# Optimization experiments

Hardware: AMD Instinct MI355X
Metric: run time of the kernel (lower is better)

Reference implementation:

```python
import jax, jax.numpy as jnp
import numpy as np

LN_EPS = 1e-5


def setup_inputs() -> dict:
    key = jax.random.key(0)
    ks = jax.random.split(key, 4)
    B, N, C, K = 512, 100, 256, 3
    query = jax.random.normal(ks[0], (B, N, C), dtype=jnp.float32)
    value = jax.random.normal(ks[1], (B, N, C), dtype=jnp.float32)
    # nn.Linear(C, N+K): weight stored as [out,in] in torch; here use [in,out]
    W_wl = jax.random.normal(ks[2], (C, N + K), dtype=jnp.float32) / np.sqrt(C)
    b_wl = jax.random.normal(ks[3], (N + K,), dtype=jnp.float32) * 0.01
    ln_gamma = jnp.ones((C,), dtype=jnp.float32)
    ln_beta = jnp.zeros((C,), dtype=jnp.float32)
    return {"query": query, "value": value, "W_wl": W_wl, "b_wl": b_wl,
            "ln_gamma": ln_gamma, "ln_beta": ln_beta}


def reference(query, value, W_wl, b_wl, ln_gamma, ln_beta):
    B, N, C = query.shape
    K = W_wl.shape[1] - N
    # dynamic conv weights from query: [B, N, K] depthwise + [B, N, N] pointwise
    dy = jnp.einsum('bnc,ck->bnk', query, W_wl) + b_wl
    dw = dy[:, :, :K]          # depthwise kernels, one per (b, proposal)
    pw = dy[:, :, K:]          # pointwise mixing matrix [B, N, N]
    # depthwise conv1d along C with 'same' padding (cross-correlation like torch)
    pad_l = (K - 1) // 2
    pad_r = K - 1 - pad_l
    vp = jnp.pad(value, ((0, 0), (0, 0), (pad_l, pad_r)))
    depth = jnp.zeros_like(value)
    for k in range(K):  # K is tiny (3): static unrolled loop
        depth = depth + dw[:, :, k:k + 1] * vp[:, :, k:k + C]
    depth = jax.nn.relu(depth)
    # pointwise conv (kernel size 1) == per-sample NxN mix over proposals
    out = jnp.einsum('bnm,bmc->bnc', pw, depth)
    # LayerNorm over C
    mu = jnp.mean(out, axis=-1, keepdims=True)
    var = jnp.var(out, axis=-1, keepdims=True)
    out = (out - mu) * jax.lax.rsqrt(var + LN_EPS) * ln_gamma + ln_beta
    return out
```

## Files before the change

### kernel.cpp

```cpp
#include <hip/hip_runtime.h>

#define NN 100
#define CC 256
#define NKK 103
#define LSA 72
#define LDPW 136
#define OTS 260

typedef __bf16 bf16;
typedef __bf16 bf16x4 __attribute__((ext_vector_type(4)));
typedef __bf16 bf16x8 __attribute__((ext_vector_type(8)));
typedef float f32x4 __attribute__((ext_vector_type(4)));

__global__ __launch_bounds__(512, 4)
void dysepconv_fused(const float* __restrict__ query,
                     const float* __restrict__ value,
                     const float* __restrict__ W,
                     const float* __restrict__ bwl,
                     const float* __restrict__ gamma,
                     const float* __restrict__ beta,
                     float* __restrict__ out)
{
    __shared__ __align__(16) bf16 PW[NN * LDPW];
    __shared__ __align__(16) bf16 R[100 * LSA + NKK * LSA];
    __shared__ float DW[NN][3];
    __shared__ float RP[8][NN][2];
    __shared__ float RS[NN][2];

    bf16*  Abuf = R;
    bf16*  Wbuf = R + 100 * LSA;
    float* OT   = (float*)R;

    const int t    = threadIdx.x;
    const int w    = t >> 6;
    const int lane = t & 63;
    const int ln16 = lane & 15;
    const int g    = lane >> 4;
    const int hi8  = g * 8;
    const int b    = blockIdx.x;

    const float* qb = query + (size_t)b * NN * CC;
    const float* vb = value + (size_t)b * NN * CC;

    f32x4 acc1[7];
    #pragma unroll
    for (int I = 0; I < 7; ++I) acc1[I] = (f32x4){0.f, 0.f, 0.f, 0.f};

    for (int kc = 0; kc < 4; ++kc) {
        const int k0 = kc * 64;
        __syncthreads();
        {
            f32x4 qv[4];
            #pragma unroll
            for (int p = 0; p < 4; ++p) {
                int idx = p * 512 + t;
                if (idx < 1600) {
                    int r = idx >> 4, j = (idx & 15) << 2;
                    qv[p] = *(const f32x4*)(qb + r * CC + k0 + j);
                }
            }
            #pragma unroll
            for (int p = 0; p < 4; ++p) {
                int idx = p * 512 + t;
                if (idx < 1600) {
                    int r = idx >> 4, j = (idx & 15) << 2;
                    bf16x4 s;
                    #pragma unroll
                    for (int i = 0; i < 4; ++i) s[i] = (bf16)qv[p][i];
                    *(bf16x4*)&Abuf[r * LSA + j] = s;
                }
            }
        }
        {
            float wv[13];
            #pragma unroll
            for (int p = 0; p < 13; ++p) {
                int idx = p * 512 + t;
                if (idx < 64 * NKK) {
                    int kk = idx / NKK, ka = idx - kk * NKK;
                    wv[p] = W[(size_t)(k0 + kk) * NKK + ka];
                }
            }
            #pragma unroll
            for (int p = 0; p < 13; ++p) {
                int idx = p * 512 + t;
                if (idx < 64 * NKK) {
                    int kk = idx / NKK, ka = idx - kk * NKK;
                    Wbuf[ka * LSA + kk] = (bf16)wv[p];
                }
            }
        }
        __syncthreads();

        if (w < 7) {
            const int rB = (w * 16 + ln16 < NKK) ? (w * 16 + ln16) : (NKK - 1);
            #pragma unroll
            for (int s = 0; s < 2; ++s) {
                bf16x8 bv = *(const bf16x8*)&Wbuf[rB * LSA + s * 32 + hi8];
                #pragma unroll
                for (int I = 0; I < 7; ++I) {
                    int row = I * 16 + ln16;
                    row = (row < NN) ? row : (NN - 1);
                    bf16x8 av = *(const bf16x8*)&Abuf[row * LSA + s * 32 + hi8];
                    acc1[I] = __builtin_amdgcn_mfma_f32_16x16x32_bf16(av, bv, acc1[I], 0, 0, 0);
                }
            }
        }
    }
    __syncthreads();

    for (int i = t; i < NN * 28; i += 512) {
        int r = i / 28, m = 100 + (i - (i / 28) * 28);
        PW[r * LDPW + m] = (bf16)0.f;
    }
    if (w < 7) {
        const int kap = w * 16 + ln16;
        const float bw = (kap < NKK) ? bwl[kap] : 0.f;
        #pragma unroll
        for (int I = 0; I < 7; ++I) {
            #pragma unroll
            for (int r = 0; r < 4; ++r) {
                int n = I * 16 + g * 4 + r;
                if (n < NN && kap < NKK) {
                    float v = acc1[I][r] + bw;
                    if (kap < 3) DW[n][kap] = v;
                    else         PW[n * LDPW + (kap - 3)] = (bf16)v;
                }
            }
        }
    }
    __syncthreads();

    f32x4 acc2[2][7];
    #pragma unroll
    for (int st = 0; st < 2; ++st)
        #pragma unroll
        for (int I = 0; I < 7; ++I) acc2[st][I] = (f32x4){0.f, 0.f, 0.f, 0.f};

    const int cb = w * 16 + ln16;
    #pragma unroll
    for (int ks = 0; ks < 4; ++ks) {
        float xv[8], yv[8];
        #pragma unroll
        for (int j = 0; j < 8; ++j) {
            int m = ks * 32 + hi8 + j;
            bool mv = (m < NN);
            const float* vr = vb + m * CC;
            xv[j] = mv ? vr[cb]       : 0.f;
            yv[j] = mv ? vr[cb + 128] : 0.f;
        }
        bf16x8 dv0, dv1;
        #pragma unroll
        for (int j = 0; j < 8; ++j) {
            int  m  = ks * 32 + hi8 + j;
            bool mv = (m < NN);
            int  mc = mv ? m : (NN - 1);
            float w0 = DW[mc][0], w1 = DW[mc][1], w2 = DW[mc][2];
            float x0 = xv[j], y0 = yv[j];
            float xm = __shfl(x0, (lane - 1) & 63), xp = __shfl(x0, (lane + 1) & 63);
            float ym = __shfl(y0, (lane - 1) & 63), yp = __shfl(y0, (lane + 1) & 63);
            if (ln16 == 0) {
                xm = (mv && cb > 0) ? vb[m * CC + cb - 1] : 0.f;
                ym = mv ? vb[m * CC + cb + 127] : 0.f;
            }
            if (ln16 == 15) {
                xp = mv ? vb[m * CC + cb + 1] : 0.f;
                yp = (mv && cb + 129 < CC) ? vb[m * CC + cb + 129] : 0.f;
            }
            float d0 = w0 * xm + w1 * x0 + w2 * xp;
            float d1 = w0 * ym + w1 * y0 + w2 * yp;
            dv0[j] = (bf16)(mv ? fmaxf(d0, 0.f) : 0.f);
            dv1[j] = (bf16)(mv ? fmaxf(d1, 0.f) : 0.f);
        }
        #pragma unroll
        for (int I = 0; I < 7; ++I) {
            int row = I * 16 + ln16;
            row = (row < NN) ? row : (NN - 1);
            bf16x8 af = *(const bf16x8*)&PW[row * LDPW + ks * 32 + hi8];
            acc2[0][I] = __builtin_amdgcn_mfma_f32_16x16x32_bf16(af, dv0, acc2[0][I], 0, 0, 0);
            acc2[1][I] = __builtin_amdgcn_mfma_f32_16x16x32_bf16(af, dv1, acc2[1][I], 0, 0, 0);
        }
    }

    #pragma unroll
    for (int I = 0; I < 7; ++I) {
        #pragma unroll
        for (int r = 0; r < 4; ++r) {
            float a = acc2[0][I][r], e = acc2[1][I][r];
            float s1 = a + e, s2 = a * a + e * e;
            #pragma unroll
            for (int mk = 1; mk < 16; mk <<= 1) {
                s1 += __shfl_xor(s1, mk);
                s2 += __shfl_xor(s2, mk);
            }
            int n = I * 16 + g * 4 + r;
            if (ln16 == 0 && n < NN) {
                RP[w][n][0] = s1;
                RP[w][n][1] = s2;
            }
        }
    }
    __syncthreads();
    if (t < NN) {
        float S1 = 0.f, S2 = 0.f;
        #pragma unroll
        for (int wi = 0; wi < 8; ++wi) { S1 += RP[wi][t][0]; S2 += RP[wi][t][1]; }
        float mu  = S1 * (1.f / 256.f);
        float var = S2 * (1.f / 256.f) - mu * mu;
        RS[t][0] = mu;
        RS[t][1] = rsqrtf(fmaxf(var, 0.f) + 1e-5f);
    }
    __syncthreads();

    const float gm0 = gamma[cb], gm1 = gamma[cb + 128];
    const float bt0 = beta[cb],  bt1 = beta[cb + 128];
    float* ob = out + (size_t)b * NN * CC;
    #pragma unroll
    for (int I = 0; I < 7; ++I) {
        #pragma unroll
        for (int r = 0; r < 4; ++r) {
            int n = I * 16 + g * 4 + r;
            if (n < NN) {
                float mu = RS[n][0], rs = RS[n][1];
                int rt = g * 4 + r;
                OT[rt * OTS + cb]       = (acc2[0][I][r] - mu) * rs * gm0 + bt0;
                OT[rt * OTS + cb + 128] = (acc2[1][I][r] - mu) * rs * gm1 + bt1;
            }
        }
        __syncthreads();
        #pragma unroll
        for (int p = 0; p < 2; ++p) {
            int idx  = p * 512 + t;
            int row  = idx >> 6, c4 = (idx & 63) << 2;
            int grow = I * 16 + row;
            if (grow < NN)
                *(f32x4*)(ob + grow * CC + c4) = *(const f32x4*)&OT[row * OTS + c4];
        }
        __syncthreads();
    }
}

extern "C" void kernel_launch(void* const* d_in, const int* in_sizes, int n_in,
                              void* d_out, int out_size, void* d_ws, size_t ws_size,
                              hipStream_t stream) {
    const float* query = (const float*)d_in[0];
    const float* value = (const float*)d_in[1];
    const float* W     = (const float*)d_in[2];
    const float* bwl   = (const float*)d_in[3];
    const float* gamma = (const float*)d_in[4];
    const float* beta  = (const float*)d_in[5];
    dysepconv_fused<<<dim3(512), dim3(512), 0, stream>>>(query, value, W, bwl, gamma, beta, (float*)d_out);
}
```

Measured before the change: 192.3 us.

## Pre-transpose weights to bf16, prefetch query/value tiles, batch output staging

A small pre-kernel transposes and converts the projection weight to bf16 in workspace, so each block loads its weight fragments straight into registers instead of re-staging them through shared memory every k-chunk. Query and value loads are software-prefetched one chunk ahead to overlap global latency with MFMA work, and the output LayerNorm write-out is staged in three 40-row batches instead of seven 16-row batches, cutting barriers. Shared memory is repacked into one manual buffer. This adds an extra kernel launch and higher register pressure from prefetch buffers.

```diff
diff --git a/kernel.cpp b/kernel.cpp
--- a/kernel.cpp
+++ b/kernel.cpp
@@ -12,24 +12,32 @@
 typedef __bf16 bf16x8 __attribute__((ext_vector_type(8)));
 typedef float f32x4 __attribute__((ext_vector_type(4)));
 
+__global__ void wl_transpose(const float* __restrict__ W, bf16* __restrict__ Wt)
+{
+    int idx = blockIdx.x * 256 + threadIdx.x;
+    if (idx < NKK * CC) {
+        int ka = idx >> 8;
+        int k  = idx & 255;
+        Wt[ka * CC + k] = (bf16)W[k * NKK + ka];
+    }
+}
+
 __global__ __launch_bounds__(512, 4)
 void dysepconv_fused(const float* __restrict__ query,
                      const float* __restrict__ value,
-                     const float* __restrict__ W,
+                     const bf16*  __restrict__ Wt,
                      const float* __restrict__ bwl,
                      const float* __restrict__ gamma,
                      const float* __restrict__ beta,
                      float* __restrict__ out)
 {
-    __shared__ __align__(16) bf16 PW[NN * LDPW];
-    __shared__ __align__(16) bf16 R[100 * LSA + NKK * LSA];
-    __shared__ float DW[NN][3];
-    __shared__ float RP[8][NN][2];
-    __shared__ float RS[NN][2];
-
-    bf16*  Abuf = R;
-    bf16*  Wbuf = R + 100 * LSA;
-    float* OT   = (float*)R;
+    __shared__ __align__(16) char SMEM[50000];
+    bf16*  PW   = (bf16*)SMEM;
+    bf16*  Abuf = (bf16*)(SMEM + 27200);
+    float (*DW)[3]      = (float(*)[3])(SMEM + 41600);
+    float (*RP)[NN][2]  = (float(*)[NN][2])(SMEM + 42800);
+    float (*RS)[2]      = (float(*)[2])(SMEM + 49200);
+    float* OT = (float*)SMEM;
 
     const int t    = threadIdx.x;
     const int w    = t >> 6;
@@ -38,6 +46,7 @@
     const int g    = lane >> 4;
     const int hi8  = g * 8;
     const int b    = blockIdx.x;
+    const int cb   = w * 16 + ln16;
 
     const float* qb = query + (size_t)b * NN * CC;
     const float* vb = value + (size_t)b * NN * CC;
@@ -46,57 +55,55 @@
     #pragma unroll
     for (int I = 0; I < 7; ++I) acc1[I] = (f32x4){0.f, 0.f, 0.f, 0.f};
 
+    const int rB = (w * 16 + ln16 < NKK) ? (w * 16 + ln16) : (NKK - 1);
+    bf16x8 wfrag[4][2];
+    #pragma unroll
+    for (int kc = 0; kc < 4; ++kc)
+        #pragma unroll
+        for (int s = 0; s < 2; ++s)
+            wfrag[kc][s] = *(const bf16x8*)(Wt + rB * CC + kc * 64 + s * 32 + hi8);
+
+    f32x4 qv[4];
+    #pragma unroll
+    for (int p = 0; p < 4; ++p) {
+        int idx = p * 512 + t;
+        if (idx < 1600) {
+            int r = idx >> 4, j = (idx & 15) << 2;
+            qv[p] = *(const f32x4*)(qb + r * CC + j);
+        }
+    }
+
+    #pragma unroll
     for (int kc = 0; kc < 4; ++kc) {
-        const int k0 = kc * 64;
-        __syncthreads();
-        {
-            f32x4 qv[4];
+        if (kc) __syncthreads();
+        #pragma unroll
+        for (int p = 0; p < 4; ++p) {
+            int idx = p * 512 + t;
+            if (idx < 1600) {
+                int r = idx >> 4, j = (idx & 15) << 2;
+                bf16x4 s;
+                #pragma unroll
+                for (int i = 0; i < 4; ++i) s[i] = (bf16)qv[p][i];
+                *(bf16x4*)&Abuf[r * LSA + j] = s;
+            }
+        }
+        f32x4 qn[4];
+        if (kc < 3) {
             #pragma unroll
             for (int p = 0; p < 4; ++p) {
                 int idx = p * 512 + t;
                 if (idx < 1600) {
                     int r = idx >> 4, j = (idx & 15) << 2;
-                    qv[p] = *(const f32x4*)(qb + r * CC + k0 + j);
-                }
-            }
-            #pragma unroll
-            for (int p = 0; p < 4; ++p) {
-                int idx = p * 512 + t;
-                if (idx < 1600) {
-                    int r = idx >> 4, j = (idx & 15) << 2;
-                    bf16x4 s;
-                    #pragma unroll
-                    for (int i = 0; i < 4; ++i) s[i] = (bf16)qv[p][i];
-                    *(bf16x4*)&Abuf[r * LSA + j] = s;
-                }
-            }
-        }
-        {
-            float wv[13];
-            #pragma unroll
-            for (int p = 0; p < 13; ++p) {
-                int idx = p * 512 + t;
-                if (idx < 64 * NKK) {
-                    int kk = idx / NKK, ka = idx - kk * NKK;
-                    wv[p] = W[(size_t)(k0 + kk) * NKK + ka];
-                }
-            }
-            #pragma unroll
-            for (int p = 0; p < 13; ++p) {
-                int idx = p * 512 + t;
-                if (idx < 64 * NKK) {
-                    int kk = idx / NKK, ka = idx - kk * NKK;
-                    Wbuf[ka * LSA + kk] = (bf16)wv[p];
+                    qn[p] = *(const f32x4*)(qb + r * CC + (kc + 1) * 64 + j);
                 }
             }
         }
         __syncthreads();
 
         if (w < 7) {
-            const int rB = (w * 16 + ln16 < NKK) ? (w * 16 + ln16) : (NKK - 1);
             #pragma unroll
             for (int s = 0; s < 2; ++s) {
-                bf16x8 bv = *(const bf16x8*)&Wbuf[rB * LSA + s * 32 + hi8];
+                bf16x8 bv = wfrag[kc][s];
                 #pragma unroll
                 for (int I = 0; I < 7; ++I) {
                     int row = I * 16 + ln16;
@@ -106,12 +113,23 @@
                 }
             }
         }
-    }
-    __syncthreads();
+        if (kc < 3) {
+            #pragma unroll
+            for (int p = 0; p < 4; ++p) qv[p] = qn[p];
+        }
+    }
 
     for (int i = t; i < NN * 28; i += 512) {
         int r = i / 28, m = 100 + (i - (i / 28) * 28);
         PW[r * LDPW + m] = (bf16)0.f;
+    }
+    float xv[8], yv[8];
+    #pragma unroll
+    for (int j = 0; j < 8; ++j) {
+        int m = hi8 + j;
+        const float* vr = vb + m * CC;
+        xv[j] = vr[cb];
+        yv[j] = vr[cb + 128];
     }
     if (w < 7) {
         const int kap = w * 16 + ln16;
@@ -137,17 +155,18 @@
         #pragma unroll
         for (int I = 0; I < 7; ++I) acc2[st][I] = (f32x4){0.f, 0.f, 0.f, 0.f};
 
-    const int cb = w * 16 + ln16;
     #pragma unroll
     for (int ks = 0; ks < 4; ++ks) {
-        float xv[8], yv[8];
-        #pragma unroll
-        for (int j = 0; j < 8; ++j) {
-            int m = ks * 32 + hi8 + j;
-            bool mv = (m < NN);
-            const float* vr = vb + m * CC;
-            xv[j] = mv ? vr[cb]       : 0.f;
-            yv[j] = mv ? vr[cb + 128] : 0.f;
+        float xn[8], yn[8];
+        if (ks < 3) {
+            #pragma unroll
+            for (int j = 0; j < 8; ++j) {
+                int m = (ks + 1) * 32 + hi8 + j;
+                bool mv = (m < NN);
+                const float* vr = vb + m * CC;
+                xn[j] = mv ? vr[cb]       : 0.f;
+                yn[j] = mv ? vr[cb + 128] : 0.f;
+            }
         }
         bf16x8 dv0, dv1;
         #pragma unroll
@@ -180,7 +199,14 @@
             acc2[0][I] = __builtin_amdgcn_mfma_f32_16x16x32_bf16(af, dv0, acc2[0][I], 0, 0, 0);
             acc2[1][I] = __builtin_amdgcn_mfma_f32_16x16x32_bf16(af, dv1, acc2[1][I], 0, 0, 0);
         }
-    }
+        if (ks < 3) {
+            #pragma unroll
+            for (int j = 0; j < 8; ++j) { xv[j] = xn[j]; yv[j] = yn[j]; }
+        }
+    }
+
+    const float gm0 = gamma[cb], gm1 = gamma[cb + 128];
+    const float bt0 = beta[cb],  bt1 = beta[cb + 128];
 
     #pragma unroll
     for (int I = 0; I < 7; ++I) {
@@ -212,31 +238,34 @@
     }
     __syncthreads();
 
-    const float gm0 = gamma[cb], gm1 = gamma[cb + 128];
-    const float bt0 = beta[cb],  bt1 = beta[cb + 128];
     float* ob = out + (size_t)b * NN * CC;
     #pragma unroll
-    for (int I = 0; I < 7; ++I) {
-        #pragma unroll
-        for (int r = 0; r < 4; ++r) {
-            int n = I * 16 + g * 4 + r;
-            if (n < NN) {
-                float mu = RS[n][0], rs = RS[n][1];
-                int rt = g * 4 + r;
-                OT[rt * OTS + cb]       = (acc2[0][I][r] - mu) * rs * gm0 + bt0;
-                OT[rt * OTS + cb + 128] = (acc2[1][I][r] - mu) * rs * gm1 + bt1;
+    for (int h = 0; h < 3; ++h) {
+        const int n0   = h * 40;
+        const int rows = (h == 2) ? 20 : 40;
+        #pragma unroll
+        for (int I = 0; I < 7; ++I) {
+            #pragma unroll
+            for (int r = 0; r < 4; ++r) {
+                int n = I * 16 + g * 4 + r;
+                if (n >= n0 && n < n0 + rows) {
+                    float mu = RS[n][0], rs = RS[n][1];
+                    int rt = n - n0;
+                    OT[rt * OTS + cb]       = (acc2[0][I][r] - mu) * rs * gm0 + bt0;
+                    OT[rt * OTS + cb + 128] = (acc2[1][I][r] - mu) * rs * gm1 + bt1;
+                }
             }
         }
         __syncthreads();
         #pragma unroll
-        for (int p = 0; p < 2; ++p) {
-            int idx  = p * 512 + t;
-            int row  = idx >> 6, c4 = (idx & 63) << 2;
-            int grow = I * 16 + row;
-            if (grow < NN)
-                *(f32x4*)(ob + grow * CC + c4) = *(const f32x4*)&OT[row * OTS + c4];
-        }
-        __syncthreads();
+        for (int p = 0; p < 5; ++p) {
+            int idx = p * 512 + t;
+            if (idx < rows * 64) {
+                int row = idx >> 6, c4 = (idx & 63) << 2;
+                *(f32x4*)(ob + (size_t)(n0 + row) * CC + c4) = *(const f32x4*)&OT[row * OTS + c4];
+            }
+        }
+        if (h < 2) __syncthreads();
     }
 }
 
@@ -249,5 +278,8 @@
     const float* bwl   = (const float*)d_in[3];
     const float* gamma = (const float*)d_in[4];
     const float* beta  = (const float*)d_in[5];
-    dysepconv_fused<<<dim3(512), dim3(512), 0, stream>>>(query, value, W, bwl, gamma, beta, (float*)d_out);
+    bf16* Wt = (bf16*)d_ws;
+
+    wl_transpose<<<dim3((NKK * CC + 255) / 256), dim3(256), 0, stream>>>(W, Wt);
+    dysepconv_fused<<<dim3(512), dim3(512), 0, stream>>>(query, value, Wt, bwl, gamma, beta, (float*)d_out);
 }
```

New measurement: 197.5 us. 1.03x slower.
